# Optimization experiments

Hardware: AMD Instinct MI355X
Metric: run time of the kernel (lower is better)

## Reference

```python
import jax, jax.numpy as jnp
import numpy as np

N = 16384          # tokens (batch*seq)
D = 2048           # input_dim
H = 2 * D          # router hidden dim
E = 64             # num_experts
NUM_SHARED = 8
TOP_K = 2


def setup_inputs() -> dict:
    key = jax.random.key(0)
    k_x, k_w1, k_b1, k_w2, k_b2 = jax.random.split(key, 5)
    s1 = 1.0 / np.sqrt(D)
    s2 = 1.0 / np.sqrt(H)
    return {
        "x": jax.random.normal(k_x, (N, D), dtype=jnp.float32),
        "W1": jax.random.uniform(k_w1, (D, H), jnp.float32, -s1, s1),
        "b1": jax.random.uniform(k_b1, (H,), jnp.float32, -s1, s1),
        "W2": jax.random.uniform(k_w2, (H, E), jnp.float32, -s2, s2),
        "b2": jax.random.uniform(k_b2, (E,), jnp.float32, -s2, s2),
    }


def reference(x, W1, b1, W2, b2):
    # router MLP: linear -> exact (erf) GELU -> linear -> softmax
    h = jax.nn.gelu(x @ W1 + b1, approximate=False)          # [N, H]
    weights = jax.nn.softmax(h @ W2 + b2, axis=-1)            # [N, E]
    global_weights = weights[:, :NUM_SHARED]                  # [N, num_shared]
    local = weights[:, NUM_SHARED:]                           # [N, E - num_shared]
    local_weights, local_indices = jax.lax.top_k(local, TOP_K)  # [N, top_k] each
    return (global_weights, local_weights, local_indices, weights)
```

## Files before the change

kernel.cpp:

```cpp
#include <hip/hip_runtime.h>
#include <math.h>

namespace {
constexpr int kN = 16384;
constexpr int kD = 2048;
constexpr int kH = 4096;
constexpr int kE = 64;
constexpr int kShared = 8;

constexpr int OFF_GW = 0;
constexpr int OFF_LW = kN * kShared;
constexpr int OFF_LI = OFF_LW + kN * 2;
constexpr int OFF_W  = OFF_LI + kN * 2;

constexpr int GS_STRIDE = 132;
constexpr int HSPLIT = 4;
constexpr int CHUNKS = 8;

constexpr size_t XH_OFF  = 0;
constexpr size_t XL_OFF  = (size_t)kN * kD;
constexpr size_t W1TH_OFF = XL_OFF + (size_t)kN * kD;
constexpr size_t W1TL_OFF = W1TH_OFF + (size_t)kH * kD;
constexpr size_t WS_BASE = (W1TL_OFF + (size_t)kH * kD) * 2;
constexpr size_t PART_FLOAT_OFF = WS_BASE / 4;
constexpr size_t WS_FULL = WS_BASE + (size_t)HSPLIT * kN * kE * 4;
}

typedef _Float16 half8  __attribute__((ext_vector_type(8)));
typedef _Float16 half4t __attribute__((ext_vector_type(4)));
typedef float    f32x16 __attribute__((ext_vector_type(16)));

__device__ __forceinline__ void async16(const _Float16* g, _Float16* l) {
    __builtin_amdgcn_global_load_lds(
        (const __attribute__((address_space(1))) void*)g,
        (__attribute__((address_space(3))) void*)l, 16, 0, 0);
}

__global__ __launch_bounds__(256)
void convert_x(const float* __restrict__ x, _Float16* __restrict__ xh,
               _Float16* __restrict__ xl)
{
    const size_t i = ((size_t)blockIdx.x * 256 + threadIdx.x) * 4;
    const float4 v = *reinterpret_cast<const float4*>(x + i);
    half4t h, l;
    const float vs[4] = {v.x, v.y, v.z, v.w};
    #pragma unroll
    for (int j = 0; j < 4; ++j) {
        const _Float16 hj = (_Float16)vs[j];
        h[j] = hj;
        l[j] = (_Float16)((vs[j] - (float)hj) * 2048.0f);
    }
    *reinterpret_cast<half4t*>(xh + i) = h;
    *reinterpret_cast<half4t*>(xl + i) = l;
}

__global__ __launch_bounds__(256)
void convert_w1t(const float* __restrict__ W1, _Float16* __restrict__ th,
                 _Float16* __restrict__ tl)
{
    __shared__ float T[64][65];
    const int bk = blockIdx.x & 31;
    const int bn = blockIdx.x >> 5;
    const int k0 = bk * 64, n0 = bn * 64;
    const int t = threadIdx.x;
    const int c4 = (t & 15) * 4, r = t >> 4;

    #pragma unroll
    for (int i = 0; i < 4; ++i) {
        const int kk = r + 16 * i;
        const float4 v = *reinterpret_cast<const float4*>(
            W1 + (size_t)(k0 + kk) * kH + n0 + c4);
        T[kk][c4 + 0] = v.x; T[kk][c4 + 1] = v.y;
        T[kk][c4 + 2] = v.z; T[kk][c4 + 3] = v.w;
    }
    __syncthreads();
    #pragma unroll
    for (int i = 0; i < 4; ++i) {
        const int nn = r + 16 * i;
        half4t h, l;
        #pragma unroll
        for (int j = 0; j < 4; ++j) {
            const float vv = T[c4 + j][nn];
            const _Float16 hj = (_Float16)vv;
            h[j] = hj;
            l[j] = (_Float16)((vv - (float)hj) * 2048.0f);
        }
        *reinterpret_cast<half4t*>(th + (size_t)(n0 + nn) * kD + k0 + c4) = h;
        *reinterpret_cast<half4t*>(tl + (size_t)(n0 + nn) * kD + k0 + c4) = l;
    }
}

__global__ __launch_bounds__(256, 2)
void gemm1_mfma(const _Float16* __restrict__ xh, const float* __restrict__ b1,
                const float* __restrict__ W2, float* __restrict__ dst,
                int atomicMode)
{
    __shared__ __align__(16) float smem[64 * GS_STRIDE];
    _Float16* lds = (_Float16*)smem;
    float* gS = smem;

    const int t = threadIdx.x;
    const int lane = t & 63;
    const int w = t >> 6;
    const int bx = blockIdx.x;
    const int hSplit = bx & 3;
    const int rowBlock = bx >> 2;
    const int rowBase = rowBlock * 128;

    const int mw = (w >> 1) * 64, nw = (w & 1) * 64;

    unsigned int gofsA[4], gofsB[4];
    #pragma unroll
    for (int i = 0; i < 8; ++i) {
        const int c = i * 256 + t;
        const int tile = c >> 9;
        const int s = c & 511;
        const int row = s >> 2;
        const int pq = s & 3;
        const int q = pq ^ (row & 3) ^ ((row >> 2) & 3);
        const unsigned int plane =
            (tile == 0) ? (unsigned int)XH_OFF :
            (tile == 1) ? (unsigned int)XL_OFF :
            (tile == 2) ? (unsigned int)W1TH_OFF : (unsigned int)W1TL_OFF;
        if (tile < 2)
            gofsA[i] = plane + (unsigned int)(rowBase + row) * kD + q * 8;
        else
            gofsB[i - 4] = plane + (unsigned int)row * kD + q * 8;
    }

    int aOff[2][2], bOff[2][2];
    #pragma unroll
    for (int mt = 0; mt < 2; ++mt)
        #pragma unroll
        for (int ks = 0; ks < 2; ++ks) {
            const int row = mw + mt * 32 + (lane & 31);
            const int q = (lane >> 5) + 2 * ks;
            aOff[mt][ks] = row * 32 + ((q ^ (row & 3) ^ ((row >> 2) & 3)) * 8);
        }
    #pragma unroll
    for (int nt = 0; nt < 2; ++nt)
        #pragma unroll
        for (int ks = 0; ks < 2; ++ks) {
            const int row = nw + nt * 32 + (lane & 31);
            const int q = (lane >> 5) + 2 * ks;
            bOff[nt][ks] = row * 32 + ((q ^ (row & 3) ^ ((row >> 2) & 3)) * 8);
        }

    const int g_r0 = (t >> 3) * 4;
    const int g_e0 = (t & 7) * 8;
    float lacc[4][8];
    #pragma unroll
    for (int i = 0; i < 4; ++i)
        #pragma unroll
        for (int j = 0; j < 8; ++j) lacc[i][j] = 0.0f;

    for (int chunk = 0; chunk < CHUNKS; ++chunk) {
        const int hBase = hSplit * (CHUNKS * 128) + chunk * 128;
        const unsigned int hOff = (unsigned int)hBase * kD;

        f32x16 accH[2][2], accL[2][2];
        #pragma unroll
        for (int a = 0; a < 2; ++a)
            #pragma unroll
            for (int b = 0; b < 2; ++b)
                #pragma unroll
                for (int r = 0; r < 16; ++r) { accH[a][b][r] = 0.0f; accL[a][b][r] = 0.0f; }

        for (int kt = 0; kt < kD; kt += 32) {
            __syncthreads();
            #pragma unroll
            for (int i = 0; i < 4; ++i)
                async16(xh + gofsA[i] + kt, lds + ((i * 256 + t) * 8));
            #pragma unroll
            for (int i = 0; i < 4; ++i)
                async16(xh + gofsB[i] + hOff + kt, lds + (((i + 4) * 256 + t) * 8));
            __syncthreads();

            half8 aH[2][2], aL[2][2], bH[2][2], bL[2][2];
            #pragma unroll
            for (int mt = 0; mt < 2; ++mt)
                #pragma unroll
                for (int ks = 0; ks < 2; ++ks) {
                    aH[mt][ks] = *reinterpret_cast<const half8*>(lds + aOff[mt][ks]);
                    aL[mt][ks] = *reinterpret_cast<const half8*>(lds + 4096 + aOff[mt][ks]);
                }
            #pragma unroll
            for (int nt = 0; nt < 2; ++nt)
                #pragma unroll
                for (int ks = 0; ks < 2; ++ks) {
                    bH[nt][ks] = *reinterpret_cast<const half8*>(lds + 8192 + bOff[nt][ks]);
                    bL[nt][ks] = *reinterpret_cast<const half8*>(lds + 12288 + bOff[nt][ks]);
                }

            #pragma unroll
            for (int ks = 0; ks < 2; ++ks)
                #pragma unroll
                for (int mt = 0; mt < 2; ++mt)
                    #pragma unroll
                    for (int nt = 0; nt < 2; ++nt) {
                        accH[mt][nt] = __builtin_amdgcn_mfma_f32_32x32x16_f16(
                            aH[mt][ks], bH[nt][ks], accH[mt][nt], 0, 0, 0);
                        accL[mt][nt] = __builtin_amdgcn_mfma_f32_32x32x16_f16(
                            aH[mt][ks], bL[nt][ks], accL[mt][nt], 0, 0, 0);
                        accL[mt][nt] = __builtin_amdgcn_mfma_f32_32x32x16_f16(
                            aL[mt][ks], bH[nt][ks], accL[mt][nt], 0, 0, 0);
                    }
        }

        const float inv2048 = 1.0f / 2048.0f;
        for (int hf = 0; hf < 2; ++hf) {
            __syncthreads();
            if ((w & 1) == hf) {
                #pragma unroll
                for (int nt = 0; nt < 2; ++nt) {
                    const int hl = nt * 32 + (lane & 31);
                    const float bb = b1[hBase + hf * 64 + hl];
                    #pragma unroll
                    for (int mt = 0; mt < 2; ++mt) {
                        #pragma unroll
                        for (int rq = 0; rq < 4; ++rq) {
                            float vr[4];
                            #pragma unroll
                            for (int rr = 0; rr < 4; ++rr) {
                                const int r = rq * 4 + rr;
                                const float hv = accH[mt][nt][r] + accL[mt][nt][r] * inv2048 + bb;
                                vr[rr] = 0.5f * hv * (1.0f + erff(hv * 0.70710678118654752f));
                            }
                            const int mrow = mw + mt * 32 + 8 * rq + 4 * (lane >> 5);
                            *reinterpret_cast<float4*>(gS + hl * GS_STRIDE + mrow) =
                                make_float4(vr[0], vr[1], vr[2], vr[3]);
                        }
                    }
                }
            }
            __syncthreads();
            const float* W2p = W2 + (size_t)(hBase + hf * 64) * kE + g_e0;
            #pragma unroll 4
            for (int h = 0; h < 64; ++h) {
                const float4 gv = *reinterpret_cast<const float4*>(gS + h * GS_STRIDE + g_r0);
                const float4 w0 = *reinterpret_cast<const float4*>(W2p + (size_t)h * kE);
                const float4 w1 = *reinterpret_cast<const float4*>(W2p + (size_t)h * kE + 4);
                const float ga[4] = {gv.x, gv.y, gv.z, gv.w};
                const float wb[8] = {w0.x, w0.y, w0.z, w0.w, w1.x, w1.y, w1.z, w1.w};
                #pragma unroll
                for (int i = 0; i < 4; ++i)
                    #pragma unroll
                    for (int j = 0; j < 8; ++j)
                        lacc[i][j] = fmaf(ga[i], wb[j], lacc[i][j]);
            }
        }
    }

    if (atomicMode) {
        #pragma unroll
        for (int i = 0; i < 4; ++i)
            #pragma unroll
            for (int j = 0; j < 8; ++j)
                atomicAdd(dst + (size_t)(rowBase + g_r0 + i) * kE + g_e0 + j, lacc[i][j]);
    } else {
        float* drow = dst + ((size_t)hSplit * kN + rowBase + g_r0) * kE + g_e0;
        #pragma unroll
        for (int i = 0; i < 4; ++i) {
            *reinterpret_cast<float4*>(drow + (size_t)i * kE) =
                make_float4(lacc[i][0], lacc[i][1], lacc[i][2], lacc[i][3]);
            *reinterpret_cast<float4*>(drow + (size_t)i * kE + 4) =
                make_float4(lacc[i][4], lacc[i][5], lacc[i][6], lacc[i][7]);
        }
    }
}

__global__ __launch_bounds__(256, 2)
void gemm1_kernel(const float* __restrict__ x, const float* __restrict__ W1,
                  const float* __restrict__ b1, const float* __restrict__ W2,
                  float* __restrict__ logits)
{
    __shared__ __align__(16) float smem[64 * GS_STRIDE];
    float* As = smem;
    float* Bs = smem + 32 * 128;
    float* gS = smem;

    const int t  = threadIdx.x;
    const int bx = blockIdx.x;
    const int rowBlock = bx >> 2;
    const int hSplit   = bx & 3;
    const int rowBase  = rowBlock * 128;
    const int hBase0   = hSplit * 1024;

    const int ty = t >> 4;
    const int tx = t & 15;
    const int r0 = ty * 8;
    const int c0 = tx * 8;
    const int g_r0 = (t >> 3) * 4;
    const int g_e0 = (t & 7) * 8;

    float lacc[4][8];
    #pragma unroll
    for (int i = 0; i < 4; ++i)
        #pragma unroll
        for (int j = 0; j < 8; ++j) lacc[i][j] = 0.0f;

    for (int chunk = 0; chunk < 8; ++chunk) {
        const int hBase = hBase0 + chunk * 128;
        float C[8][8];
        #pragma unroll
        for (int i = 0; i < 8; ++i)
            #pragma unroll
            for (int j = 0; j < 8; ++j) C[i][j] = 0.0f;

        for (int kt = 0; kt < kD; kt += 32) {
            __syncthreads();
            #pragma unroll
            for (int i = 0; i < 4; ++i) {
                const int f  = t + 256 * i;
                const int m  = f >> 3;
                const int kq = (f & 7) * 4;
                const float4 v = *reinterpret_cast<const float4*>(
                    x + (size_t)(rowBase + m) * kD + kt + kq);
                As[(kq + 0) * 128 + m] = v.x;
                As[(kq + 1) * 128 + m] = v.y;
                As[(kq + 2) * 128 + m] = v.z;
                As[(kq + 3) * 128 + m] = v.w;
            }
            #pragma unroll
            for (int i = 0; i < 4; ++i) {
                const int f  = t + 256 * i;
                const int k  = f >> 5;
                const int n4 = (f & 31) * 4;
                *reinterpret_cast<float4*>(Bs + k * 128 + n4) =
                    *reinterpret_cast<const float4*>(W1 + (size_t)(kt + k) * kH + hBase + n4);
            }
            __syncthreads();
            #pragma unroll 8
            for (int k = 0; k < 32; ++k) {
                const float4 a0 = *reinterpret_cast<const float4*>(As + k * 128 + r0);
                const float4 a1 = *reinterpret_cast<const float4*>(As + k * 128 + r0 + 4);
                const float4 b0 = *reinterpret_cast<const float4*>(Bs + k * 128 + c0);
                const float4 b1v = *reinterpret_cast<const float4*>(Bs + k * 128 + c0 + 4);
                const float a[8] = {a0.x, a0.y, a0.z, a0.w, a1.x, a1.y, a1.z, a1.w};
                const float b[8] = {b0.x, b0.y, b0.z, b0.w, b1v.x, b1v.y, b1v.z, b1v.w};
                #pragma unroll
                for (int i = 0; i < 8; ++i)
                    #pragma unroll
                    for (int j = 0; j < 8; ++j)
                        C[i][j] = fmaf(a[i], b[j], C[i][j]);
            }
        }

        #pragma unroll
        for (int j = 0; j < 8; ++j) {
            const float bb = b1[hBase + c0 + j];
            #pragma unroll
            for (int i = 0; i < 8; ++i) {
                const float hv = C[i][j] + bb;
                C[i][j] = 0.5f * hv * (1.0f + erff(hv * 0.70710678118654752f));
            }
        }

        for (int half = 0; half < 2; ++half) {
            __syncthreads();
            if ((tx >> 3) == half) {
                const int hloc0 = c0 - half * 64;
                #pragma unroll
                for (int j = 0; j < 8; ++j) {
                    const float4 col = make_float4(C[0][j], C[1][j], C[2][j], C[3][j]);
                    const float4 col2 = make_float4(C[4][j], C[5][j], C[6][j], C[7][j]);
                    *reinterpret_cast<float4*>(gS + (hloc0 + j) * GS_STRIDE + r0)     = col;
                    *reinterpret_cast<float4*>(gS + (hloc0 + j) * GS_STRIDE + r0 + 4) = col2;
                }
            }
            __syncthreads();
            const float* W2p = W2 + (size_t)(hBase + half * 64) * kE + g_e0;
            #pragma unroll 4
            for (int h = 0; h < 64; ++h) {
                const float4 gv = *reinterpret_cast<const float4*>(gS + h * GS_STRIDE + g_r0);
                const float4 w0 = *reinterpret_cast<const float4*>(W2p + (size_t)h * kE);
                const float4 w1 = *reinterpret_cast<const float4*>(W2p + (size_t)h * kE + 4);
                const float ga[4] = {gv.x, gv.y, gv.z, gv.w};
                const float wb[8] = {w0.x, w0.y, w0.z, w0.w, w1.x, w1.y, w1.z, w1.w};
                #pragma unroll
                for (int i = 0; i < 4; ++i)
                    #pragma unroll
                    for (int j = 0; j < 8; ++j)
                        lacc[i][j] = fmaf(ga[i], wb[j], lacc[i][j]);
            }
        }
    }

    #pragma unroll
    for (int i = 0; i < 4; ++i)
        #pragma unroll
        for (int j = 0; j < 8; ++j)
            atomicAdd(logits + (size_t)(rowBase + g_r0 + i) * kE + g_e0 + j, lacc[i][j]);
}

__global__ __launch_bounds__(256)
void router_kernel(const float* __restrict__ b2, const float* __restrict__ src,
                   int atomicMode, float* __restrict__ out)
{
    const int lane = threadIdx.x & 63;
    const int row  = blockIdx.x * 4 + (threadIdx.x >> 6);

    float logit;
    if (atomicMode) {
        logit = src[(size_t)row * kE + lane] + b2[lane];
    } else {
        const float* p = src + (size_t)row * kE + lane;
        logit = p[0] + p[(size_t)kN * kE] + p[(size_t)2 * kN * kE] +
                p[(size_t)3 * kN * kE] + b2[lane];
    }

    float m = logit;
    #pragma unroll
    for (int off = 32; off > 0; off >>= 1) m = fmaxf(m, __shfl_xor(m, off));
    const float p = expf(logit - m);
    float s = p;
    #pragma unroll
    for (int off = 32; off > 0; off >>= 1) s += __shfl_xor(s, off);
    const float w = p / s;

    out[OFF_W + (size_t)row * kE + lane] = w;
    if (lane < kShared) out[OFF_GW + (size_t)row * kShared + lane] = w;

    float v1 = (lane >= kShared) ? w : -1.0f;
    int   i1 = lane - kShared;
    #pragma unroll
    for (int off = 32; off > 0; off >>= 1) {
        const float ov = __shfl_xor(v1, off);
        const int   oi = __shfl_xor(i1, off);
        if (ov > v1 || (ov == v1 && oi < i1)) { v1 = ov; i1 = oi; }
    }
    float v2 = (lane >= kShared && (lane - kShared) != i1) ? w : -1.0f;
    int   i2 = lane - kShared;
    #pragma unroll
    for (int off = 32; off > 0; off >>= 1) {
        const float ov = __shfl_xor(v2, off);
        const int   oi = __shfl_xor(i2, off);
        if (ov > v2 || (ov == v2 && oi < i2)) { v2 = ov; i2 = oi; }
    }
    if (lane == 0) {
        out[OFF_LW + (size_t)row * 2 + 0] = v1;
        out[OFF_LW + (size_t)row * 2 + 1] = v2;
        out[OFF_LI + (size_t)row * 2 + 0] = (float)i1;
        out[OFF_LI + (size_t)row * 2 + 1] = (float)i2;
    }
}

extern "C" void kernel_launch(void* const* d_in, const int* in_sizes, int n_in,
                              void* d_out, int out_size, void* d_ws, size_t ws_size,
                              hipStream_t stream)
{
    const float* x  = (const float*)d_in[0];
    const float* W1 = (const float*)d_in[1];
    const float* b1 = (const float*)d_in[2];
    const float* W2 = (const float*)d_in[3];
    const float* b2 = (const float*)d_in[4];
    float* out = (float*)d_out;
    float* logits = out + OFF_W;

    if (ws_size >= WS_BASE) {
        _Float16* base = (_Float16*)d_ws;
        const int atomicMode = (ws_size >= WS_FULL) ? 0 : 1;
        float* dst = atomicMode ? logits : ((float*)d_ws + PART_FLOAT_OFF);
        if (atomicMode)
            hipMemsetAsync(logits, 0, (size_t)kN * kE * sizeof(float), stream);
        hipLaunchKernelGGL(convert_x, dim3(kN * kD / 1024), dim3(256), 0, stream,
                           x, base + XH_OFF, base + XL_OFF);
        hipLaunchKernelGGL(convert_w1t, dim3((kD / 64) * (kH / 64)), dim3(256), 0, stream,
                           W1, base + W1TH_OFF, base + W1TL_OFF);
        hipLaunchKernelGGL(gemm1_mfma, dim3((kN / 128) * HSPLIT), dim3(256), 0, stream,
                           base + XH_OFF, b1, W2, dst, atomicMode);
        hipLaunchKernelGGL(router_kernel, dim3(kN / 4), dim3(256), 0, stream,
                           b2, dst, atomicMode, out);
    } else {
        hipMemsetAsync(logits, 0, (size_t)kN * kE * sizeof(float), stream);
        hipLaunchKernelGGL(gemm1_kernel, dim3((kN / 128) * 4), dim3(256), 0, stream,
                           x, W1, b1, W2, logits);
        hipLaunchKernelGGL(router_kernel, dim3(kN / 4), dim3(256), 0, stream,
                           b2, logits, 1, out);
    }
}
```

Baseline: 1.307 ms.

## Double-buffer LDS tiles in gemm1 to overlap async loads with MFMA

Doubles the shared-memory allocation and prefetches the next K-tile (crossing chunk boundaries) into the alternate buffer with async global-to-LDS loads while MFMAs run on the current one. Replaces the __syncthreads pairs with explicit vmcnt/lgkmcnt waits and raw s_barrier. The GELU/W2 epilogue reuses the just-consumed buffer while the next chunk's first tile is in flight. This aims to hide global load latency, at the cost of twice the LDS per block, which can limit occupancy, and more fragile hand-managed wait counts.

Result: no change. 1.291 ms (-1.2%).

```diff
diff --git a/kernel.cpp b/kernel.cpp
--- a/kernel.cpp
+++ b/kernel.cpp
@@ -24,6 +24,9 @@
 constexpr size_t WS_BASE = (W1TL_OFF + (size_t)kH * kD) * 2;
 constexpr size_t PART_FLOAT_OFF = WS_BASE / 4;
 constexpr size_t WS_FULL = WS_BASE + (size_t)HSPLIT * kN * kE * 4;
+
+constexpr int BUF_FLOATS = 64 * GS_STRIDE;
+constexpr int BUF_F16    = BUF_FLOATS * 2;
 }
 
 typedef _Float16 half8  __attribute__((ext_vector_type(8)));
@@ -95,9 +98,7 @@
                 const float* __restrict__ W2, float* __restrict__ dst,
                 int atomicMode)
 {
-    __shared__ __align__(16) float smem[64 * GS_STRIDE];
-    _Float16* lds = (_Float16*)smem;
-    float* gS = smem;
+    __shared__ __align__(16) float smem[2 * BUF_FLOATS];
 
     const int t = threadIdx.x;
     const int lane = t & 63;
@@ -154,9 +155,23 @@
         #pragma unroll
         for (int j = 0; j < 8; ++j) lacc[i][j] = 0.0f;
 
+    auto stage = [&](int buf, int chunk, int kt) {
+        _Float16* l = (_Float16*)smem + (size_t)buf * BUF_F16;
+        const unsigned int hOff =
+            (unsigned int)(hSplit * (CHUNKS * 128) + chunk * 128) * kD;
+        #pragma unroll
+        for (int i = 0; i < 4; ++i)
+            async16(xh + gofsA[i] + kt, l + ((i * 256 + t) * 8));
+        #pragma unroll
+        for (int i = 0; i < 4; ++i)
+            async16(xh + gofsB[i] + hOff + kt, l + (((i + 4) * 256 + t) * 8));
+    };
+
+    int cur = 0;
+    stage(0, 0, 0);
+
     for (int chunk = 0; chunk < CHUNKS; ++chunk) {
         const int hBase = hSplit * (CHUNKS * 128) + chunk * 128;
-        const unsigned int hOff = (unsigned int)hBase * kD;
 
         f32x16 accH[2][2], accL[2][2];
         #pragma unroll
@@ -167,14 +182,19 @@
                 for (int r = 0; r < 16; ++r) { accH[a][b][r] = 0.0f; accL[a][b][r] = 0.0f; }
 
         for (int kt = 0; kt < kD; kt += 32) {
-            __syncthreads();
-            #pragma unroll
-            for (int i = 0; i < 4; ++i)
-                async16(xh + gofsA[i] + kt, lds + ((i * 256 + t) * 8));
-            #pragma unroll
-            for (int i = 0; i < 4; ++i)
-                async16(xh + gofsB[i] + hOff + kt, lds + (((i + 4) * 256 + t) * 8));
-            __syncthreads();
+            const bool isLast = (chunk == CHUNKS - 1) && (kt == kD - 32);
+            if (!isLast) {
+                int nc = chunk, nk = kt + 32;
+                if (nk == kD) { nc = chunk + 1; nk = 0; }
+                stage(cur ^ 1, nc, nk);
+                asm volatile("s_waitcnt vmcnt(8)" ::: "memory");
+            } else {
+                asm volatile("s_waitcnt vmcnt(0)" ::: "memory");
+            }
+            __builtin_amdgcn_s_barrier();
+            asm volatile("" ::: "memory");
+
+            const _Float16* lds = (const _Float16*)smem + (size_t)cur * BUF_F16;
 
             half8 aH[2][2], aL[2][2], bH[2][2], bL[2][2];
             #pragma unroll
@@ -205,11 +225,18 @@
                         accL[mt][nt] = __builtin_amdgcn_mfma_f32_32x32x16_f16(
                             aL[mt][ks], bH[nt][ks], accL[mt][nt], 0, 0, 0);
                     }
-        }
-
+
+            asm volatile("s_waitcnt lgkmcnt(0)" ::: "memory");
+            __builtin_amdgcn_s_barrier();
+            cur ^= 1;
+        }
+
+        float* gS = smem + (size_t)(cur ^ 1) * BUF_FLOATS;
         const float inv2048 = 1.0f / 2048.0f;
         for (int hf = 0; hf < 2; ++hf) {
-            __syncthreads();
+            asm volatile("s_waitcnt lgkmcnt(0)" ::: "memory");
+            __builtin_amdgcn_s_barrier();
+            asm volatile("" ::: "memory");
             if ((w & 1) == hf) {
                 #pragma unroll
                 for (int nt = 0; nt < 2; ++nt) {
@@ -233,7 +260,9 @@
                     }
                 }
             }
-            __syncthreads();
+            asm volatile("s_waitcnt lgkmcnt(0)" ::: "memory");
+            __builtin_amdgcn_s_barrier();
+            asm volatile("" ::: "memory");
             const float* W2p = W2 + (size_t)(hBase + hf * 64) * kE + g_e0;
             #pragma unroll 4
             for (int h = 0; h < 64; ++h) {
@@ -249,6 +278,8 @@
                         lacc[i][j] = fmaf(ga[i], wb[j], lacc[i][j]);
             }
         }
+        asm volatile("s_waitcnt lgkmcnt(0)" ::: "memory");
+        __builtin_amdgcn_s_barrier();
     }
 
     if (atomicMode) {
```
